# Performance work log

Measured on AMD Instinct MI355X. Metric: run time of the kernel, lower is better.

## Reference

```python
import math
import jax, jax.numpy as jnp
import numpy as np

B, H, N, L = 16, 256, 64, 4096
DT_MIN, DT_MAX = 1e-3, 1e-1


def setup_inputs() -> dict:
    key = jax.random.key(0)
    ks = jax.random.split(key, 5)
    u = jax.random.normal(ks[0], (B, H, L), dtype=jnp.float32)
    # log_dt ~ U[log(dt_min), log(dt_max)] as in __init__
    log_dt = jax.random.uniform(ks[1], (H,), dtype=jnp.float32) * (
        math.log(DT_MAX) - math.log(DT_MIN)) + math.log(DT_MIN)
    # C is a complex randn stored as real view (H, N, 2)
    C = jax.random.normal(ks[2], (H, N, 2), dtype=jnp.float32)
    log_A_real = jnp.log(0.5 * jnp.ones((H, N), dtype=jnp.float32))
    A_imag = math.pi * jnp.broadcast_to(jnp.arange(N, dtype=jnp.float32), (H, N))
    D = jax.random.normal(ks[3], (H,), dtype=jnp.float32)
    length = jax.random.randint(ks[4], (B,), 1, L + 1, dtype=jnp.int32)
    return {"u": u, "log_dt": log_dt, "C": C, "log_A_real": log_A_real,
            "A_imag": A_imag, "D": D, "length": length}


def _get_kernel(log_dt, C, log_A_real, A_imag, length):
    dt = jnp.exp(log_dt)                           # (H,)
    Cc = C[..., 0] + 1j * C[..., 1]                # (H, N) complex
    A = -jnp.exp(log_A_real) + 1j * A_imag         # (H, N)
    dtA = A * dt[:, None]                          # (H, N)
    Ct = Cc * (jnp.exp(dtA) - 1.0) / A             # (H, N)
    # Vandermonde: exp(dtA * l) for l in [0, L)  -> (H, N, L) complex
    P = dtA[:, :, None] * jnp.arange(length, dtype=jnp.float32)
    K = 2.0 * jnp.einsum('hn,hnl->hl', Ct, jnp.exp(P)).real  # (H, L)
    return K


def reference(u, log_dt, C, log_A_real, A_imag, D, length):
    # u: (B, H, L) real; length: (B,) int, per-example valid length (<= L)
    Bq, Hq, Lq = u.shape
    K = _get_kernel(log_dt, C, log_A_real, A_imag, Lq)  # (H, L)
    # Causal linear convolution via zero-padded FFT of size 2L.
    # Per-group FFT with n=2*l truncated to :l equals the causal conv y[t] =
    # sum_{s<=t} K[s] * u[t-s], which for t < length[b] only touches u[:, :t+1];
    # so one full-length FFT + length mask reproduces the grouped loop exactly.
    n = 2 * Lq
    kf = jnp.fft.rfft(K, n=n)                       # (H, L+1)
    uf = jnp.fft.rfft(u, n=n)                       # (B, H, L+1)
    y = jnp.fft.irfft(uf * kf[None], n=n)[..., :Lq]  # (B, H, L)
    y = y + u * D[:, None]
    mask = (jnp.arange(Lq)[None, :] < length[:, None]).astype(u.dtype)  # (B, L)
    return y * mask[:, None, :]
```

## Files before the change

### kernel.cpp

```cpp
#include <hip/hip_runtime.h>


#define B_SZ 16
#define H_SZ 256
#define L_SZ 4096

using s16x8 = __attribute__((ext_vector_type(8))) short;
using h16x8 = __attribute__((ext_vector_type(8))) _Float16;
using f32x4 = __attribute__((ext_vector_type(4))) float;

template <typename T>
__device__ inline auto mfma_try(T a, T b, f32x4 c, int)
    -> decltype(__builtin_amdgcn_mfma_f32_16x16x32_f16(a, b, c, 0, 0, 0)) {
  return __builtin_amdgcn_mfma_f32_16x16x32_f16(a, b, c, 0, 0, 0);
}
template <typename T>
__device__ inline f32x4 mfma_try(T a, T b, f32x4 c, long) {
  return __builtin_amdgcn_mfma_f32_16x16x32_f16(
      __builtin_bit_cast(h16x8, a), __builtin_bit_cast(h16x8, b), c, 0, 0, 0);
}
__device__ inline f32x4 MFMA(s16x8 a, s16x8 b, f32x4 c) {
  return mfma_try(a, b, c, 0);
}

__device__ inline unsigned short f2h(float f) {
  return __builtin_bit_cast(unsigned short, (_Float16)f);
}

#define O_U   0
#define O_VR  8192
#define O_VI  16384
#define O_XR  O_VR
#define O_XI  O_VI
#define O_TT  24576
#define O_GR  32768
#define O_GM  40960
#define O_BR  49152
#define O_BI  65536
#define O_K   O_BR
#define LDS_TOTAL 81920

#define MATS_SHORTS_PER_H (5 * 4096)
#define WS_MATS_BYTES ((size_t)H_SZ * MATS_SHORTS_PER_H * 2)
#define WS_LAM_OFF    WS_MATS_BYTES
#define WS_NEEDED     (WS_MATS_BYTES + (size_t)H_SZ * 64 * 2 * 4)

__global__ __launch_bounds__(256) void dssm_setup(
    const float* __restrict__ log_dt,
    const float* __restrict__ Cin,
    const float* __restrict__ log_A_real,
    const float* __restrict__ A_imag,
    unsigned short* __restrict__ mats,
    float* __restrict__ lam)
{
  __shared__ unsigned short sm[5 * 4096];
  __shared__ float sKs[64];
  const int tid = threadIdx.x;
  const int l = tid & 63;
  const int wv = tid >> 6;
  const int h = blockIdx.x;

  const float dt = expf(log_dt[h]);
  const float ar = expf(log_A_real[h * 64 + l]);
  const float ai = A_imag[h * 64 + l];
  const float er = expf(-ar * dt);
  const float th = ai * dt;
  const float wr = er * cosf(th), wi = er * sinf(th);
  const float em1r = wr - 1.0f, em1i = wi;
  const float inv = 1.0f / (ar * ar + ai * ai);
  const float qr = (em1i * ai - em1r * ar) * inv;
  const float qi = -(em1r * ai + em1i * ar) * inv;
  const float c0 = Cin[(h * 64 + l) * 2 + 0];
  const float c1 = Cin[(h * 64 + l) * 2 + 1];
  const float c2r = 2.0f * (c0 * qr - c1 * qi);
  const float c2i = 2.0f * (c0 * qi + c1 * qr);

  const float w2r = wr*wr - wi*wi,     w2i = 2.f*wr*wi;
  const float w4r = w2r*w2r - w2i*w2i, w4i = 2.f*w2r*w2i;
  const float w8r = w4r*w4r - w4i*w4i, w8i = 2.f*w4r*w4i;
  const float w16r= w8r*w8r - w8i*w8i, w16i= 2.f*w8r*w8i;

  float b0r = 1.f, b0i = 0.f;
  for (int s2 = 0; s2 < wv; ++s2) {
    const float nr = b0r*w16r - b0i*w16i, ni = b0r*w16i + b0i*w16r;
    b0r = nr; b0i = ni;
  }

  {
    float pr = b0r, pi = b0i;
    #pragma unroll
    for (int kk = 0; kk < 16; ++kk) {
      const int k = wv * 16 + kk;
      sm[0 * 4096 + l * 64 + (63 - k)] = f2h(pr);
      sm[1 * 4096 + l * 64 + (63 - k)] = f2h(pi);
      const float nr = pr*wr - pi*wi, ni = pr*wi + pi*wr;
      pr = nr; pi = ni;
    }
  }

  {
    float pr = b0r, pi = b0i;
    #pragma unroll
    for (int kk = 0; kk < 16; ++kk) {
      const int k = 16*wv + kk;
      const float gre = c2r*pr - c2i*pi;
      const float gim = c2r*pi + c2i*pr;
      float s = gre;
      #pragma unroll
      for (int m = 1; m < 64; m <<= 1) s += __shfl_xor(s, m, 64);
      if (l == 0) sKs[k] = s;
      if (k >= 1) {
        sm[3 * 4096 + (k - 1) * 64 + l] = f2h(gre);
        sm[4 * 4096 + (k - 1) * 64 + l] = f2h(-gim);
      }
      const float nr = pr*wr - pi*wi, ni = pr*wi + pi*wr;
      pr = nr; pi = ni;
    }
    if (wv == 3) {
      const float gre = c2r*pr - c2i*pi;
      const float gim = c2r*pi + c2i*pr;
      sm[3 * 4096 + 63 * 64 + l] = f2h(gre);
      sm[4 * 4096 + 63 * 64 + l] = f2h(-gim);
      lam[(h * 64 + l) * 2 + 0] = pr;
      lam[(h * 64 + l) * 2 + 1] = pi;
    }
  }
  __syncthreads();

  {
    const int tau = tid >> 2;
    const int sb = (tid & 3) * 16;
    #pragma unroll
    for (int e = 0; e < 16; ++e) {
      const int s = sb + e;
      const float kv = (s <= tau) ? sKs[tau - s] : 0.0f;
      sm[2 * 4096 + tau * 64 + s] = f2h(kv);
    }
  }
  __syncthreads();

  unsigned short* dst = mats + (size_t)h * MATS_SHORTS_PER_H;
  #pragma unroll
  for (int i = 0; i < 10; ++i) {
    const int c = i * 256 + tid;
    *(s16x8*)(dst + c * 8) = *(const s16x8*)(sm + c * 8);
  }
}

__global__ __launch_bounds__(256) void dssm_main(
    const float* __restrict__ u,
    const unsigned short* __restrict__ mats,
    const float* __restrict__ lam,
    const float* __restrict__ Dvec,
    const int* __restrict__ length,
    float* __restrict__ y)
{
  extern __shared__ char smem[];
  float* sBr = (float*)(smem + O_BR);
  float* sBi = (float*)(smem + O_BI);

  const int tid = threadIdx.x;
  const int l = tid & 63;
  const int wv = tid >> 6;
  const int h = blockIdx.x & 255;
  const int b = blockIdx.x >> 8;
  const size_t base = ((size_t)b * H_SZ + h) * L_SZ;
  const float* up = u + base;

  const float Dh = Dvec[h];
  const int len = length[b];
  const float lr = lam[(h * 64 + l) * 2 + 0];
  const float li = lam[(h * 64 + l) * 2 + 1];

  {
    const int e0 = tid * 16;
    const float4 f0 = *(const float4*)(up + e0);
    const float4 f1 = *(const float4*)(up + e0 + 4);
    const float4 f2 = *(const float4*)(up + e0 + 8);
    const float4 f3 = *(const float4*)(up + e0 + 12);
    s16x8 v0, v1;
    v0[0]=(short)f2h(f0.x); v0[1]=(short)f2h(f0.y);
    v0[2]=(short)f2h(f0.z); v0[3]=(short)f2h(f0.w);
    v0[4]=(short)f2h(f1.x); v0[5]=(short)f2h(f1.y);
    v0[6]=(short)f2h(f1.z); v0[7]=(short)f2h(f1.w);
    v1[0]=(short)f2h(f2.x); v1[1]=(short)f2h(f2.y);
    v1[2]=(short)f2h(f2.z); v1[3]=(short)f2h(f2.w);
    v1[4]=(short)f2h(f3.x); v1[5]=(short)f2h(f3.y);
    v1[6]=(short)f2h(f3.z); v1[7]=(short)f2h(f3.w);
    const int r = tid >> 2;
    const int q0 = (2 * tid) & 7;
    char* ub = smem + O_U + r * 128;
    *(s16x8*)(ub + (((q0    ) ^ (r & 7)) << 4)) = v0;
    *(s16x8*)(ub + (((q0 + 1) ^ (r & 7)) << 4)) = v1;
  }

  {
    const unsigned short* mb = mats + (size_t)h * MATS_SHORTS_PER_H;
    const int r = tid >> 2;
    const int q0 = (2 * tid) & 7;
    const int rsw = r & 7;
    #pragma unroll
    for (int m = 0; m < 5; ++m) {
      const s16x8 va = *(const s16x8*)(mb + m * 4096 + tid * 16);
      const s16x8 vb = *(const s16x8*)(mb + m * 4096 + tid * 16 + 8);
      char* bs = smem + 8192 + m * 8192 + r * 128;
      *(s16x8*)(bs + (((q0    ) ^ rsw) << 4)) = va;
      *(s16x8*)(bs + (((q0 + 1) ^ rsw) << 4)) = vb;
    }
  }
  __syncthreads();

  auto frag = [&](int base_, int row, int kc) -> s16x8 {
    return *(const s16x8*)(smem + base_ + row * 128 + ((kc ^ (row & 7)) << 4));
  };
  const int arow = 16 * wv + (l & 15);
  const int kq = l >> 4;
  const s16x8 aU0 = frag(O_U, arow, kq);
  const s16x8 aU1 = frag(O_U, arow, 4 + kq);

  {
    f32x4 accR[4], accI[4];
    #pragma unroll
    for (int j = 0; j < 4; ++j) { accR[j] = f32x4{0,0,0,0}; accI[j] = f32x4{0,0,0,0}; }
    #pragma unroll
    for (int j = 0; j < 4; ++j) {
      const int bcol = 16 * j + (l & 15);
      accR[j] = MFMA(aU0, frag(O_VR, bcol, kq),     accR[j]);
      accR[j] = MFMA(aU1, frag(O_VR, bcol, 4 + kq), accR[j]);
      accI[j] = MFMA(aU0, frag(O_VI, bcol, kq),     accI[j]);
      accI[j] = MFMA(aU1, frag(O_VI, bcol, 4 + kq), accI[j]);
    }
    #pragma unroll
    for (int j = 0; j < 4; ++j) {
      const int n = 16 * j + (l & 15);
      #pragma unroll
      for (int r = 0; r < 4; ++r) {
        const int c = 16 * wv + (l >> 4) * 4 + r;
        sBr[c * 64 + n] = accR[j][r];
        sBi[c * 64 + n] = accI[j][r];
      }
    }
  }
  __syncthreads();

  if (wv == 0) {
    float xr = 0.f, xi = 0.f;
    #pragma unroll 4
    for (int c = 0; c < 64; ++c) {
      const int xo = c * 128 + (((l >> 3) ^ (c & 7)) << 4) + (l & 7) * 2;
      *(unsigned short*)(smem + O_XR + xo) = f2h(xr);
      *(unsigned short*)(smem + O_XI + xo) = f2h(xi);
      const float br = sBr[c*64 + l];
      const float bi = sBi[c*64 + l];
      const float nr = fmaf(lr, xr, fmaf(-li, xi, br));
      const float ni = fmaf(lr, xi, fmaf(li, xr, bi));
      xr = nr; xi = ni;
    }
  }
  __syncthreads();

  f32x4 accT[4], accX[4];
  #pragma unroll
  for (int j = 0; j < 4; ++j) { accT[j] = f32x4{0,0,0,0}; accX[j] = f32x4{0,0,0,0}; }
  const s16x8 aXr0 = frag(O_XR, arow, kq);
  const s16x8 aXr1 = frag(O_XR, arow, 4 + kq);
  const s16x8 aXi0 = frag(O_XI, arow, kq);
  const s16x8 aXi1 = frag(O_XI, arow, 4 + kq);
  #pragma unroll
  for (int j = 0; j < 4; ++j) {
    const int bcol = 16 * j + (l & 15);
    accT[j] = MFMA(aU0,  frag(O_TT, bcol, kq),     accT[j]);
    accT[j] = MFMA(aU1,  frag(O_TT, bcol, 4 + kq), accT[j]);
    accX[j] = MFMA(aXr0, frag(O_GR, bcol, kq),     accX[j]);
    accX[j] = MFMA(aXr1, frag(O_GR, bcol, 4 + kq), accX[j]);
    accX[j] = MFMA(aXi0, frag(O_GM, bcol, kq),     accX[j]);
    accX[j] = MFMA(aXi1, frag(O_GM, bcol, 4 + kq), accX[j]);
  }

  float* yp = y + base;
  #pragma unroll
  for (int j = 0; j < 4; ++j) {
    #pragma unroll
    for (int r = 0; r < 4; ++r) {
      const int t = (16 * wv + (l >> 4) * 4 + r) * 64 + 16 * j + (l & 15);
      const float out = fmaf(Dh, up[t], accT[j][r] + accX[j][r]);
      yp[t] = (t < len) ? out : 0.0f;
    }
  }
}

__global__ __launch_bounds__(256) void dssm_fb(
    const float* __restrict__ u,
    const float* __restrict__ log_dt,
    const float* __restrict__ Cin,
    const float* __restrict__ log_A_real,
    const float* __restrict__ A_imag,
    const float* __restrict__ Dvec,
    const int* __restrict__ length,
    float* __restrict__ y)
{
  extern __shared__ char smem[];
  float* sBr = (float*)(smem + O_BR);
  float* sBi = (float*)(smem + O_BI);
  float* sK  = (float*)(smem + O_K);

  const int tid = threadIdx.x;
  const int l = tid & 63;
  const int wv = tid >> 6;
  const int h = blockIdx.x & 255;
  const int b = blockIdx.x >> 8;
  const size_t base = ((size_t)b * H_SZ + h) * L_SZ;
  const float* up = u + base;

  const float dt = expf(log_dt[h]);
  const float ar = expf(log_A_real[h * 64 + l]);
  const float ai = A_imag[h * 64 + l];
  const float er = expf(-ar * dt);
  const float th = ai * dt;
  const float wr = er * cosf(th), wi = er * sinf(th);
  const float em1r = wr - 1.0f, em1i = wi;
  const float inv = 1.0f / (ar * ar + ai * ai);
  const float qr = (em1i * ai - em1r * ar) * inv;
  const float qi = -(em1r * ai + em1i * ar) * inv;
  const float c0 = Cin[(h * 64 + l) * 2 + 0];
  const float c1 = Cin[(h * 64 + l) * 2 + 1];
  const float c2r = 2.0f * (c0 * qr - c1 * qi);
  const float c2i = 2.0f * (c0 * qi + c1 * qr);

  const float w2r = wr*wr - wi*wi,     w2i = 2.f*wr*wi;
  const float w4r = w2r*w2r - w2i*w2i, w4i = 2.f*w2r*w2i;
  const float w8r = w4r*w4r - w4i*w4i, w8i = 2.f*w4r*w4i;
  const float w16r= w8r*w8r - w8i*w8i, w16i= 2.f*w8r*w8i;

  float b0r = 1.f, b0i = 0.f;
  for (int s2 = 0; s2 < wv; ++s2) {
    const float nr = b0r*w16r - b0i*w16i, ni = b0r*w16i + b0i*w16r;
    b0r = nr; b0i = ni;
  }

  {
    const int e0 = tid * 16;
    const float4 f0 = *(const float4*)(up + e0);
    const float4 f1 = *(const float4*)(up + e0 + 4);
    const float4 f2 = *(const float4*)(up + e0 + 8);
    const float4 f3 = *(const float4*)(up + e0 + 12);
    s16x8 v0, v1;
    v0[0]=(short)f2h(f0.x); v0[1]=(short)f2h(f0.y);
    v0[2]=(short)f2h(f0.z); v0[3]=(short)f2h(f0.w);
    v0[4]=(short)f2h(f1.x); v0[5]=(short)f2h(f1.y);
    v0[6]=(short)f2h(f1.z); v0[7]=(short)f2h(f1.w);
    v1[0]=(short)f2h(f2.x); v1[1]=(short)f2h(f2.y);
    v1[2]=(short)f2h(f2.z); v1[3]=(short)f2h(f2.w);
    v1[4]=(short)f2h(f3.x); v1[5]=(short)f2h(f3.y);
    v1[6]=(short)f2h(f3.z); v1[7]=(short)f2h(f3.w);
    const int r = tid >> 2;
    const int q0 = (2 * tid) & 7;
    char* ub = smem + O_U + r * 128;
    *(s16x8*)(ub + (((q0    ) ^ (r & 7)) << 4)) = v0;
    *(s16x8*)(ub + (((q0 + 1) ^ (r & 7)) << 4)) = v1;
  }
  {
    float pr = b0r, pi = b0i;
    #pragma unroll
    for (int kk = 0; kk < 16; ++kk) {
      const int k = wv * 16 + kk;
      const int c63 = 63 - k;
      const int vb = l * 128 + (((c63 >> 3) ^ (l & 7)) << 4) + (c63 & 7) * 2;
      *(unsigned short*)(smem + O_VR + vb) = f2h(pr);
      *(unsigned short*)(smem + O_VI + vb) = f2h(pi);
      const float nr = pr*wr - pi*wi, ni = pr*wi + pi*wr;
      pr = nr; pi = ni;
    }
  }
  {
    float pr = b0r, pi = b0i;
    #pragma unroll
    for (int kk = 0; kk < 16; ++kk) {
      const int k = 16*wv + kk;
      const float gre = c2r*pr - c2i*pi;
      const float gim = c2r*pi + c2i*pr;
      float s = gre;
      #pragma unroll
      for (int m = 1; m < 64; m <<= 1) s += __shfl_xor(s, m, 64);
      if (l == 0) sK[k] = s;
      if (k >= 1) {
        const int row = k - 1;
        const int gb = row * 128 + (((l >> 3) ^ (row & 7)) << 4) + (l & 7) * 2;
        *(unsigned short*)(smem + O_GR + gb) = f2h(gre);
        *(unsigned short*)(smem + O_GM + gb) = f2h(-gim);
      }
      const float nr = pr*wr - pi*wi, ni = pr*wi + pi*wr;
      pr = nr; pi = ni;
    }
    if (wv == 3) {
      const float gre = c2r*pr - c2i*pi;
      const float gim = c2r*pi + c2i*pr;
      const int gb = 63 * 128 + (((l >> 3) ^ 7) << 4) + (l & 7) * 2;
      *(unsigned short*)(smem + O_GR + gb) = f2h(gre);
      *(unsigned short*)(smem + O_GM + gb) = f2h(-gim);
    }
  }
  __syncthreads();
  {
    const int tau = tid >> 2;
    const int sb = tid & 3;
    #pragma unroll
    for (int half = 0; half < 2; ++half) {
      const int q = sb * 2 + half;
      s16x8 v;
      #pragma unroll
      for (int e = 0; e < 8; ++e) {
        const int s = q * 8 + e;
        float kv = 0.0f;
        if (s <= tau) kv = sK[tau - s];
        v[e] = (short)f2h(kv);
      }
      *(s16x8*)(smem + O_TT + tau * 128 + ((q ^ (tau & 7)) << 4)) = v;
    }
  }
  __syncthreads();

  auto frag = [&](int base_, int row, int kc) -> s16x8 {
    return *(const s16x8*)(smem + base_ + row * 128 + ((kc ^ (row & 7)) << 4));
  };
  const int arow = 16 * wv + (l & 15);
  const int kq = l >> 4;
  const s16x8 aU0 = frag(O_U, arow, kq);
  const s16x8 aU1 = frag(O_U, arow, 4 + kq);

  {
    f32x4 accR[4], accI[4];
    #pragma unroll
    for (int j = 0; j < 4; ++j) { accR[j] = f32x4{0,0,0,0}; accI[j] = f32x4{0,0,0,0}; }
    #pragma unroll
    for (int j = 0; j < 4; ++j) {
      const int bcol = 16 * j + (l & 15);
      accR[j] = MFMA(aU0, frag(O_VR, bcol, kq),     accR[j]);
      accR[j] = MFMA(aU1, frag(O_VR, bcol, 4 + kq), accR[j]);
      accI[j] = MFMA(aU0, frag(O_VI, bcol, kq),     accI[j]);
      accI[j] = MFMA(aU1, frag(O_VI, bcol, 4 + kq), accI[j]);
    }
    #pragma unroll
    for (int j = 0; j < 4; ++j) {
      const int n = 16 * j + (l & 15);
      #pragma unroll
      for (int r = 0; r < 4; ++r) {
        const int c = 16 * wv + (l >> 4) * 4 + r;
        sBr[c * 64 + n] = accR[j][r];
        sBi[c * 64 + n] = accI[j][r];
      }
    }
  }
  __syncthreads();

  if (wv == 0) {
    const float l2r = w16r*w16r - w16i*w16i, l2i = 2.f*w16r*w16i;
    const float lr  = l2r*l2r - l2i*l2i,     li  = 2.f*l2r*l2i;
    float xr = 0.f, xi = 0.f;
    #pragma unroll 4
    for (int c = 0; c < 64; ++c) {
      const int xo = c * 128 + (((l >> 3) ^ (c & 7)) << 4) + (l & 7) * 2;
      *(unsigned short*)(smem + O_XR + xo) = f2h(xr);
      *(unsigned short*)(smem + O_XI + xo) = f2h(xi);
      const float br = sBr[c*64 + l];
      const float bi = sBi[c*64 + l];
      const float nr = fmaf(lr, xr, fmaf(-li, xi, br));
      const float ni = fmaf(lr, xi, fmaf(li, xr, bi));
      xr = nr; xi = ni;
    }
  }
  __syncthreads();

  f32x4 accT[4], accX[4];
  #pragma unroll
  for (int j = 0; j < 4; ++j) { accT[j] = f32x4{0,0,0,0}; accX[j] = f32x4{0,0,0,0}; }
  const s16x8 aXr0 = frag(O_XR, arow, kq);
  const s16x8 aXr1 = frag(O_XR, arow, 4 + kq);
  const s16x8 aXi0 = frag(O_XI, arow, kq);
  const s16x8 aXi1 = frag(O_XI, arow, 4 + kq);
  #pragma unroll
  for (int j = 0; j < 4; ++j) {
    const int bcol = 16 * j + (l & 15);
    accT[j] = MFMA(aU0,  frag(O_TT, bcol, kq),     accT[j]);
    accT[j] = MFMA(aU1,  frag(O_TT, bcol, 4 + kq), accT[j]);
    accX[j] = MFMA(aXr0, frag(O_GR, bcol, kq),     accX[j]);
    accX[j] = MFMA(aXr1, frag(O_GR, bcol, 4 + kq), accX[j]);
    accX[j] = MFMA(aXi0, frag(O_GM, bcol, kq),     accX[j]);
    accX[j] = MFMA(aXi1, frag(O_GM, bcol, 4 + kq), accX[j]);
  }

  const float Dh = Dvec[h];
  const int len = length[b];
  float* yp = y + base;
  #pragma unroll
  for (int j = 0; j < 4; ++j) {
    #pragma unroll
    for (int r = 0; r < 4; ++r) {
      const int t = (16 * wv + (l >> 4) * 4 + r) * 64 + 16 * j + (l & 15);
      const float out = fmaf(Dh, up[t], accT[j][r] + accX[j][r]);
      yp[t] = (t < len) ? out : 0.0f;
    }
  }
}

extern "C" void kernel_launch(void* const* d_in, const int* in_sizes, int n_in,
                              void* d_out, int out_size, void* d_ws, size_t ws_size,
                              hipStream_t stream) {
  const float* u          = (const float*)d_in[0];
  const float* log_dt     = (const float*)d_in[1];
  const float* C          = (const float*)d_in[2];
  const float* log_A_real = (const float*)d_in[3];
  const float* A_imag     = (const float*)d_in[4];
  const float* D          = (const float*)d_in[5];
  const int*   length     = (const int*)d_in[6];
  float* y = (float*)d_out;

  if (ws_size >= WS_NEEDED && d_ws != nullptr) {
    unsigned short* mats = (unsigned short*)d_ws;
    float* lam = (float*)((char*)d_ws + WS_LAM_OFF);
    dssm_setup<<<H_SZ, 256, 0, stream>>>(log_dt, C, log_A_real, A_imag,
                                         mats, lam);
    dssm_main<<<B_SZ * H_SZ, 256, LDS_TOTAL, stream>>>(u, mats, lam, D,
                                                       length, y);
  } else {
    dssm_fb<<<B_SZ * H_SZ, 256, LDS_TOTAL, stream>>>(
        u, log_dt, C, log_A_real, A_imag, D, length, y);
  }
}
```

Baseline: 63.41 us.

## Pre-swizzle setup matrices and load them via direct global-to-LDS DMA; overlap T-matmul with scan

The setup kernel now writes the five per-head fp16 matrices in the XOR-swizzled LDS layout, so the main kernel can copy them straight into shared memory with global_load_lds instead of going through registers. Waves 1-3 compute the Toeplitz MFMA product while wave 0 runs the serial complex recurrence, and wave 0 does its share afterwards. The u values for the D skip term are also loaded into registers before the final MFMAs. This aims to hide global latency and the idle time of the serial scan, but relies on global_load_lds addressing matching the swizzled layout and adds register pressure.

```diff
diff --git a/kernel.cpp b/kernel.cpp
--- a/kernel.cpp
+++ b/kernel.cpp
@@ -59,6 +59,7 @@
   const int l = tid & 63;
   const int wv = tid >> 6;
   const int h = blockIdx.x;
+  char* smb = (char*)sm;
 
   const float dt = expf(log_dt[h]);
   const float ar = expf(log_A_real[h * 64 + l]);
@@ -91,8 +92,10 @@
     #pragma unroll
     for (int kk = 0; kk < 16; ++kk) {
       const int k = wv * 16 + kk;
-      sm[0 * 4096 + l * 64 + (63 - k)] = f2h(pr);
-      sm[1 * 4096 + l * 64 + (63 - k)] = f2h(pi);
+      const int c63 = 63 - k;
+      const int vb = l * 128 + (((c63 >> 3) ^ (l & 7)) << 4) + (c63 & 7) * 2;
+      *(unsigned short*)(smb + 0 * 8192 + vb) = f2h(pr);
+      *(unsigned short*)(smb + 1 * 8192 + vb) = f2h(pi);
       const float nr = pr*wr - pi*wi, ni = pr*wi + pi*wr;
       pr = nr; pi = ni;
     }
@@ -110,8 +113,10 @@
       for (int m = 1; m < 64; m <<= 1) s += __shfl_xor(s, m, 64);
       if (l == 0) sKs[k] = s;
       if (k >= 1) {
-        sm[3 * 4096 + (k - 1) * 64 + l] = f2h(gre);
-        sm[4 * 4096 + (k - 1) * 64 + l] = f2h(-gim);
+        const int row = k - 1;
+        const int gb = row * 128 + (((l >> 3) ^ (row & 7)) << 4) + (l & 7) * 2;
+        *(unsigned short*)(smb + 3 * 8192 + gb) = f2h(gre);
+        *(unsigned short*)(smb + 4 * 8192 + gb) = f2h(-gim);
       }
       const float nr = pr*wr - pi*wi, ni = pr*wi + pi*wr;
       pr = nr; pi = ni;
@@ -119,8 +124,9 @@
     if (wv == 3) {
       const float gre = c2r*pr - c2i*pi;
       const float gim = c2r*pi + c2i*pr;
-      sm[3 * 4096 + 63 * 64 + l] = f2h(gre);
-      sm[4 * 4096 + 63 * 64 + l] = f2h(-gim);
+      const int gb = 63 * 128 + (((l >> 3) ^ 7) << 4) + (l & 7) * 2;
+      *(unsigned short*)(smb + 3 * 8192 + gb) = f2h(gre);
+      *(unsigned short*)(smb + 4 * 8192 + gb) = f2h(-gim);
       lam[(h * 64 + l) * 2 + 0] = pr;
       lam[(h * 64 + l) * 2 + 1] = pi;
     }
@@ -129,12 +135,18 @@
 
   {
     const int tau = tid >> 2;
-    const int sb = (tid & 3) * 16;
-    #pragma unroll
-    for (int e = 0; e < 16; ++e) {
-      const int s = sb + e;
-      const float kv = (s <= tau) ? sKs[tau - s] : 0.0f;
-      sm[2 * 4096 + tau * 64 + s] = f2h(kv);
+    const int sb = tid & 3;
+    #pragma unroll
+    for (int half = 0; half < 2; ++half) {
+      const int q = sb * 2 + half;
+      s16x8 v;
+      #pragma unroll
+      for (int e = 0; e < 8; ++e) {
+        const int s = q * 8 + e;
+        const float kv = (s <= tau) ? sKs[tau - s] : 0.0f;
+        v[e] = (short)f2h(kv);
+      }
+      *(s16x8*)(smb + 2 * 8192 + tau * 128 + ((q ^ (tau & 7)) << 4)) = v;
     }
   }
   __syncthreads();
@@ -171,6 +183,17 @@
   const int len = length[b];
   const float lr = lam[(h * 64 + l) * 2 + 0];
   const float li = lam[(h * 64 + l) * 2 + 1];
+
+  {
+    const unsigned short* mb = mats + (size_t)h * MATS_SHORTS_PER_H;
+    for (int g = wv; g < 40; g += 4) {
+      const unsigned short* src = mb + g * 512 + l * 8;
+      __builtin_amdgcn_global_load_lds(
+          (const __attribute__((address_space(1))) void*)src,
+          (__attribute__((address_space(3))) void*)(smem + 8192 + g * 1024),
+          16, 0, 0);
+    }
+  }
 
   {
     const int e0 = tid * 16;
@@ -193,21 +216,6 @@
     *(s16x8*)(ub + (((q0    ) ^ (r & 7)) << 4)) = v0;
     *(s16x8*)(ub + (((q0 + 1) ^ (r & 7)) << 4)) = v1;
   }
-
-  {
-    const unsigned short* mb = mats + (size_t)h * MATS_SHORTS_PER_H;
-    const int r = tid >> 2;
-    const int q0 = (2 * tid) & 7;
-    const int rsw = r & 7;
-    #pragma unroll
-    for (int m = 0; m < 5; ++m) {
-      const s16x8 va = *(const s16x8*)(mb + m * 4096 + tid * 16);
-      const s16x8 vb = *(const s16x8*)(mb + m * 4096 + tid * 16 + 8);
-      char* bs = smem + 8192 + m * 8192 + r * 128;
-      *(s16x8*)(bs + (((q0    ) ^ rsw) << 4)) = va;
-      *(s16x8*)(bs + (((q0 + 1) ^ rsw) << 4)) = vb;
-    }
-  }
   __syncthreads();
 
   auto frag = [&](int base_, int row, int kc) -> s16x8 {
@@ -243,6 +251,17 @@
   }
   __syncthreads();
 
+  f32x4 accT[4];
+  #pragma unroll
+  for (int j = 0; j < 4; ++j) accT[j] = f32x4{0,0,0,0};
+  auto do_accT = [&]() {
+    #pragma unroll
+    for (int j = 0; j < 4; ++j) {
+      const int bcol = 16 * j + (l & 15);
+      accT[j] = MFMA(aU0, frag(O_TT, bcol, kq),     accT[j]);
+      accT[j] = MFMA(aU1, frag(O_TT, bcol, 4 + kq), accT[j]);
+    }
+  };
   if (wv == 0) {
     float xr = 0.f, xi = 0.f;
     #pragma unroll 4
@@ -256,12 +275,25 @@
       const float ni = fmaf(lr, xi, fmaf(li, xr, bi));
       xr = nr; xi = ni;
     }
-  }
-  __syncthreads();
-
-  f32x4 accT[4], accX[4];
-  #pragma unroll
-  for (int j = 0; j < 4; ++j) { accT[j] = f32x4{0,0,0,0}; accX[j] = f32x4{0,0,0,0}; }
+  } else {
+    do_accT();
+  }
+  __syncthreads();
+
+  float ureg[16];
+  #pragma unroll
+  for (int j = 0; j < 4; ++j) {
+    #pragma unroll
+    for (int r = 0; r < 4; ++r) {
+      ureg[j * 4 + r] = up[(16 * wv + (l >> 4) * 4 + r) * 64 + 16 * j + (l & 15)];
+    }
+  }
+
+  if (wv == 0) do_accT();
+
+  f32x4 accX[4];
+  #pragma unroll
+  for (int j = 0; j < 4; ++j) accX[j] = f32x4{0,0,0,0};
   const s16x8 aXr0 = frag(O_XR, arow, kq);
   const s16x8 aXr1 = frag(O_XR, arow, 4 + kq);
   const s16x8 aXi0 = frag(O_XI, arow, kq);
@@ -269,8 +301,6 @@
   #pragma unroll
   for (int j = 0; j < 4; ++j) {
     const int bcol = 16 * j + (l & 15);
-    accT[j] = MFMA(aU0,  frag(O_TT, bcol, kq),     accT[j]);
-    accT[j] = MFMA(aU1,  frag(O_TT, bcol, 4 + kq), accT[j]);
     accX[j] = MFMA(aXr0, frag(O_GR, bcol, kq),     accX[j]);
     accX[j] = MFMA(aXr1, frag(O_GR, bcol, 4 + kq), accX[j]);
     accX[j] = MFMA(aXi0, frag(O_GM, bcol, kq),     accX[j]);
@@ -283,7 +313,7 @@
     #pragma unroll
     for (int r = 0; r < 4; ++r) {
       const int t = (16 * wv + (l >> 4) * 4 + r) * 64 + 16 * j + (l & 15);
-      const float out = fmaf(Dh, up[t], accT[j][r] + accX[j][r]);
+      const float out = fmaf(Dh, ureg[j * 4 + r], accT[j][r] + accX[j][r]);
       yp[t] = (t < len) ? out : 0.0f;
     }
   }
```

New measurement: 63.09 us, median of 2. About the same (-0.5%).
